# Optimization experiments

Measured on AMD Instinct MI355X. Metric: run time of the kernel, lower is better.

Reference implementation:

```python
import jax, jax.numpy as jnp
import numpy as np

B, P, N, H = 8, 12, 5000, 8
E = 50000
NB = 8
TD0, TD1 = 16, 64
MAX_STEPS = 500


def _proj(x, w1, b1, w2, b2):
    # Projection: Linear -> ReLU -> Linear
    return jax.nn.relu(x @ w1 + b1) @ w2 + b2


def _ln(x, w, b, eps=1e-5):
    # LayerNorm over last two dims [N, H] with affine params [N, H]
    m = jnp.mean(x, axis=(-2, -1), keepdims=True)
    v = jnp.mean((x - m) ** 2, axis=(-2, -1), keepdims=True)
    return (x - m) * jax.lax.rsqrt(v + eps) * w + b


def _time_table():
    # DiffTimeEmbedding buffer: [MAX_STEPS, 2*TD0]
    steps = jnp.arange(MAX_STEPS, dtype=jnp.float32)[:, None]
    dims = jnp.arange(TD0, dtype=jnp.float32)[None, :]
    e = steps * 10.0 ** (dims * 4.0 / TD0)
    return jnp.concatenate([jnp.sin(e), jnp.cos(e)], axis=1)


def setup_inputs() -> dict:
    key = jax.random.key(0)
    ks = jax.random.split(key, 40)
    rn = lambda k, s, sc=0.1: jax.random.normal(k, s, jnp.float32) * sc
    return {
        'x': jax.random.normal(ks[0], (B, P, N), jnp.float32),
        'cond': jax.random.normal(ks[1], (B, P, N, H), jnp.float32),
        'pos': jax.random.normal(ks[2], (N, H), jnp.float32),
        'time': jax.random.randint(ks[3], (B,), 0, MAX_STEPS),
        'edge_index': jax.random.randint(ks[4], (2, E), 0, N),
        'te_w1': rn(ks[5], (2 * TD0, TD1)), 'te_b1': rn(ks[6], (TD1,)),
        'te_w2': rn(ks[7], (TD1, TD1)), 'te_b2': rn(ks[8], (TD1,)),
        'in_w1': rn(ks[9], (1, H)), 'in_b1': rn(ks[10], (H,)),
        'in_w2': rn(ks[11], (H, H)), 'in_b2': rn(ks[12], (H,)),
        'pos_w1': rn(ks[13], (H, H)), 'pos_b1': rn(ks[14], (H,)),
        'pos_w2': rn(ks[15], (H, H)), 'pos_b2': rn(ks[16], (H,)),
        'attn': jax.random.normal(ks[17], (NB + 1, 1), jnp.float32),
        'bt_w1': rn(ks[18], (NB, TD1, H)), 'bt_b1': rn(ks[19], (NB, H)),
        'bt_w2': rn(ks[20], (NB, H, H)), 'bt_b2': rn(ks[21], (NB, H)),
        'bc_w1': rn(ks[22], (NB, H, H)), 'bc_b1': rn(ks[23], (NB, H)),
        'bc_w2': rn(ks[24], (NB, H, H)), 'bc_b2': rn(ks[25], (NB, H)),
        'gn_w': 1.0 + rn(ks[26], (NB, N, H), 0.05), 'gn_b': rn(ks[27], (NB, N, H), 0.05),
        'tn_w': 1.0 + rn(ks[28], (NB, N, H), 0.05), 'tn_b': rn(ks[29], (NB, N, H), 0.05),
        'cv_w': rn(ks[30], (NB, P, P)), 'cv_b': rn(ks[31], (NB, P)),
        'out_w1': rn(ks[32], (H, H)), 'out_b1': rn(ks[33], (H,)),
        'out_w2': rn(ks[34], (H, 1)), 'out_b2': rn(ks[35], (1,)),
    }


def _forward(x, cond, pos, te_w1, te_b1, te_w2, te_b2, in_w1, in_b1, in_w2, in_b2,
             pos_w1, pos_b1, pos_w2, pos_b2, attn, bt_w1, bt_b1, bt_w2, bt_b2,
             bc_w1, bc_b1, bc_w2, bc_b2, gn_w, gn_b, tn_w, tn_b, cv_w, cv_b,
             out_w1, out_b1, out_w2, out_b2, time, edge_index):
    # diffusion-time embedding -> [B, TD1]
    te = _time_table()[time]
    te = jax.nn.silu(te @ te_w1 + te_b1)
    te = jax.nn.silu(te @ te_w2 + te_b2)
    # input + positional projection -> [B, P, N, H]
    h = _proj(x[..., None], in_w1, in_b1, in_w2, in_b2)
    h = h + _proj(pos, pos_w1, pos_b1, pos_w2, pos_b2)
    # LGConv symmetric GCN norm (no self loops), shared across blocks
    src, dst = edge_index[0], edge_index[1]
    deg = jnp.zeros((N,), h.dtype).at[dst].add(1.0)
    dinv = jnp.where(deg > 0, 1.0 / jnp.sqrt(jnp.where(deg > 0, deg, 1.0)), 0.0)
    enorm = dinv[src] * dinv[dst]  # [E]
    skips = [h]
    for i in range(NB):
        t = _proj(te, bt_w1[i], bt_b1[i], bt_w2[i], bt_b2[i])[:, None, None, :]
        c = _proj(cond, bc_w1[i], bc_b1[i], bc_w2[i], bc_b2[i])
        h = _ln(h + c, gn_w[i], gn_b[i])
        # LGConv: gather -> scale -> scatter-add along node dim (-2)
        msg = h[:, :, src, :] * enorm[None, None, :, None]
        h = jnp.zeros_like(h).at[:, :, dst, :].add(msg)
        h = _ln(h + t, tn_w[i], tn_b[i])
        # 1x1 Conv2d over period channels
        h = jnp.einsum('bpnh,qp->bqnh', h, cv_w[i]) + cv_b[i][None, :, None, None]
        skips.append(h)
    s = jnp.stack(skips, axis=-1)  # [B, P, N, H, NB+1]
    a = jax.nn.softmax(attn, axis=0)  # [NB+1, 1]
    h = (s @ a)[..., 0]  # [B, P, N, H]
    return _proj(h, out_w1, out_b1, out_w2, out_b2)[..., 0]  # [B, P, N]


def reference(x, cond, pos, te_w1, te_b1, te_w2, te_b2, in_w1, in_b1, in_w2, in_b2,
              pos_w1, pos_b1, pos_w2, pos_b2, attn, bt_w1, bt_b1, bt_w2, bt_b2,
              bc_w1, bc_b1, bc_w2, bc_b2, gn_w, gn_b, tn_w, tn_b, cv_w, cv_b,
              out_w1, out_b1, out_w2, out_b2, time, edge_index):
    return _forward(x, cond, pos, te_w1, te_b1, te_w2, te_b2, in_w1, in_b1, in_w2, in_b2,
                    pos_w1, pos_b1, pos_w2, pos_b2, attn, bt_w1, bt_b1, bt_w2, bt_b2,
                    bc_w1, bc_b1, bc_w2, bc_b2, gn_w, gn_b, tn_w, tn_b, cv_w, cv_b,
                    out_w1, out_b1, out_w2, out_b2, time, edge_index)
```

## Files before the change

### kernel.cpp

```cpp
#include <hip/hip_runtime.h>
#include <math.h>

#define Bv 8
#define Pv 12
#define Nv 5000
#define Hv 8
#define Ev 50000
#define NBv 8
#define TD1v 64
#define NIMG (Bv * Pv)
#define BLKS_PER_IMG 20
#define ECAP 3072

typedef float f4v __attribute__((ext_vector_type(4)));

__device__ inline float4 nt_load4(const float* p) {
  f4v v = __builtin_nontemporal_load((const f4v*)p);
  return make_float4(v.x, v.y, v.z, v.w);
}
__device__ inline void nt_store4(float* p, float a, float b, float c, float d) {
  f4v v = {a, b, c, d};
  __builtin_nontemporal_store(v, (f4v*)p);
}

__device__ __constant__ float POW10Q[16] = {
  1.0f, 1.7782794100389228f, 3.1622776601683795f, 5.623413251903491f,
  10.0f, 17.78279410038923f, 31.622776601683793f, 56.23413251903491f,
  100.0f, 177.82794100389228f, 316.22776601683796f, 562.341325190349f,
  1000.0f, 1778.2794100389228f, 3162.2776601683795f, 5623.413251903491f
};

__global__ void k_setup(const int* timei, const float* attn,
                        const float* te_w1, const float* te_b1,
                        const float* te_w2, const float* te_b2,
                        const float* bt_w1, const float* bt_b1,
                        const float* bt_w2, const float* bt_b2,
                        float* t_all, float* a9) {
  __shared__ float te0[Bv][32];
  __shared__ float te1[Bv][64];
  __shared__ float te2[Bv][64];
  int t = threadIdx.x;
  for (int idx = t; idx < Bv * 16; idx += 64) {
    int b = idx >> 4, d = idx & 15;
    float e = (float)timei[b] * POW10Q[d];
    te0[b][d]      = (float)sin((double)e);
    te0[b][d + 16] = (float)cos((double)e);
  }
  __syncthreads();
  for (int idx = t; idx < Bv * 64; idx += 64) {
    int b = idx >> 6, j = idx & 63;
    float s = te_b1[j];
    for (int k = 0; k < 32; ++k) s += te0[b][k] * te_w1[k * 64 + j];
    te1[b][j] = s / (1.0f + expf(-s));
  }
  __syncthreads();
  for (int idx = t; idx < Bv * 64; idx += 64) {
    int b = idx >> 6, j = idx & 63;
    float s = te_b2[j];
    for (int k = 0; k < 64; ++k) s += te1[b][k] * te_w2[k * 64 + j];
    te2[b][j] = s / (1.0f + expf(-s));
  }
  __syncthreads();
  {
    int i = t >> 3, b = t & 7;
    float u[Hv];
    for (int j = 0; j < Hv; ++j) {
      float s = bt_b1[i * Hv + j];
      for (int k = 0; k < TD1v; ++k) s += te2[b][k] * bt_w1[(i * TD1v + k) * Hv + j];
      u[j] = fmaxf(s, 0.0f);
    }
    for (int ch = 0; ch < Hv; ++ch) {
      float s = bt_b2[i * Hv + ch];
      for (int j = 0; j < Hv; ++j) s += u[j] * bt_w2[(i * Hv + j) * Hv + ch];
      t_all[(i * Bv + b) * Hv + ch] = s;
    }
  }
  if (t == 0) {
    float m = attn[0];
    for (int i = 1; i < 9; ++i) m = fmaxf(m, attn[i]);
    float s = 0.f, ex[9];
    for (int i = 0; i < 9; ++i) { ex[i] = expf(attn[i] - m); s += ex[i]; }
    for (int i = 0; i < 9; ++i) a9[i] = ex[i] / s;
  }
}

__global__ void k_posp(const float* pos, const float* pw1, const float* pb1,
                       const float* pw2, const float* pb2, float* posp) {
  int n = blockIdx.x * blockDim.x + threadIdx.x;
  if (n >= Nv) return;
  const float4* pr = (const float4*)(pos + (size_t)n * Hv);
  float4 r0 = pr[0], r1 = pr[1];
  float x[8] = {r0.x, r0.y, r0.z, r0.w, r1.x, r1.y, r1.z, r1.w};
  float u[8];
  #pragma unroll
  for (int j = 0; j < 8; ++j) {
    float s = pb1[j];
    #pragma unroll
    for (int k = 0; k < 8; ++k) s += x[k] * pw1[k * 8 + j];
    u[j] = fmaxf(s, 0.f);
  }
  float o[8];
  #pragma unroll
  for (int ch = 0; ch < 8; ++ch) {
    float s = pb2[ch];
    #pragma unroll
    for (int j = 0; j < 8; ++j) s += u[j] * pw2[j * 8 + ch];
    o[ch] = s;
  }
  float4* po = (float4*)(posp + (size_t)n * Hv);
  po[0] = make_float4(o[0], o[1], o[2], o[3]);
  po[1] = make_float4(o[4], o[5], o[6], o[7]);
}

__global__ void k_zero(float* deg, int* cursor, float* stats) {
  int i = blockIdx.x * blockDim.x + threadIdx.x;
  if (i < Nv) { deg[i] = 0.f; cursor[i] = 0; }
  if (i < NBv * 2 * NIMG * 2) stats[i] = 0.f;
}

__global__ void k_deg(const int* eidx, float* deg) {
  int e = blockIdx.x * blockDim.x + threadIdx.x;
  if (e < Ev) atomicAdd(&deg[eidx[Ev + e]], 1.0f);
}

__global__ void k_dinv(const float* deg, float* dinv) {
  int n = blockIdx.x * blockDim.x + threadIdx.x;
  if (n < Nv) {
    float d = deg[n];
    dinv[n] = d > 0.f ? (float)(1.0 / sqrt((double)d)) : 0.f;
  }
}

__global__ void k_scan(const float* deg, int* row_ptr) {
  __shared__ int buf[1024];
  __shared__ int base_s;
  int t = threadIdx.x;
  if (t == 0) { base_s = 0; row_ptr[0] = 0; }
  __syncthreads();
  for (int c = 0; c < 5; ++c) {
    int i = c * 1024 + t;
    int v = (i < Nv) ? (int)(deg[i] + 0.5f) : 0;
    buf[t] = v;
    __syncthreads();
    for (int off = 1; off < 1024; off <<= 1) {
      int add = (t >= off) ? buf[t - off] : 0;
      __syncthreads();
      buf[t] += add;
      __syncthreads();
    }
    int base = base_s;
    if (i < Nv) row_ptr[i + 1] = base + buf[t];
    __syncthreads();
    if (t == 1023) base_s = base + buf[1023];
    __syncthreads();
  }
}

__global__ void k_csr(const int* eidx, const float* dinv, const int* row_ptr,
                      int* cursor, float2* epack) {
  int e = blockIdx.x * blockDim.x + threadIdx.x;
  if (e >= Ev) return;
  int s = eidx[e], d = eidx[Ev + e];
  int slot = atomicAdd(&cursor[d], 1);
  int pos = row_ptr[d] + slot;
  epack[pos] = make_float2(__int_as_float(s), dinv[s] * dinv[d]);
}

__global__ __launch_bounds__(256) void k_gwb(
    const int* __restrict__ row_ptr, const float2* __restrict__ epack,
    const float* __restrict__ gn_w, const float* __restrict__ gn_b,
    float* __restrict__ Gw, float* __restrict__ Gb) {
  int id = blockIdx.x * 256 + threadIdx.x;
  if (id >= NBv * Nv) return;
  int i = id / Nv, n = id % Nv;
  const float* gw = gn_w + (size_t)i * Nv * Hv;
  const float* gb = gn_b + (size_t)i * Nv * Hv;
  float aw[8] = {0,0,0,0,0,0,0,0}, ab[8] = {0,0,0,0,0,0,0,0};
  int e0 = row_ptr[n], e1 = row_ptr[n + 1];
  for (int e = e0; e < e1; ++e) {
    float2 ep = epack[e];
    int s = __float_as_int(ep.x);
    float w = ep.y;
    const float4* wr = (const float4*)(gw + (size_t)s * Hv);
    const float4* br = (const float4*)(gb + (size_t)s * Hv);
    float4 w0 = wr[0], w1 = wr[1], b0 = br[0], b1 = br[1];
    aw[0] += w * w0.x; aw[1] += w * w0.y; aw[2] += w * w0.z; aw[3] += w * w0.w;
    aw[4] += w * w1.x; aw[5] += w * w1.y; aw[6] += w * w1.z; aw[7] += w * w1.w;
    ab[0] += w * b0.x; ab[1] += w * b0.y; ab[2] += w * b0.z; ab[3] += w * b0.w;
    ab[4] += w * b1.x; ab[5] += w * b1.y; ab[6] += w * b1.z; ab[7] += w * b1.w;
  }
  float4* wo = (float4*)(Gw + (size_t)id * Hv);
  wo[0] = make_float4(aw[0], aw[1], aw[2], aw[3]);
  wo[1] = make_float4(aw[4], aw[5], aw[6], aw[7]);
  float4* bo = (float4*)(Gb + (size_t)id * Hv);
  bo[0] = make_float4(ab[0], ab[1], ab[2], ab[3]);
  bo[1] = make_float4(ab[4], ab[5], ab[6], ab[7]);
}

__global__ void k_init(const float* x, const float* posp,
                       const float* iw1, const float* ib1,
                       const float* iw2, const float* ib2,
                       const float* a9, float* hA, float* acc) {
  int t = blockIdx.x * blockDim.x + threadIdx.x;
  if (t >= Bv * Pv * Nv) return;
  float xv = __builtin_nontemporal_load(x + t);
  float u[8];
  #pragma unroll
  for (int j = 0; j < 8; ++j) u[j] = fmaxf(xv * iw1[j] + ib1[j], 0.f);
  int n = t % Nv;
  const float4* pp = (const float4*)(posp + (size_t)n * Hv);
  float4 p0 = pp[0], p1 = pp[1];
  float pv[8] = {p0.x, p0.y, p0.z, p0.w, p1.x, p1.y, p1.z, p1.w};
  float a0 = a9[0];
  float o[8];
  #pragma unroll
  for (int ch = 0; ch < 8; ++ch) {
    float s = ib2[ch];
    #pragma unroll
    for (int j = 0; j < 8; ++j) s += u[j] * iw2[j * 8 + ch];
    o[ch] = s + pv[ch];
  }
  float4* hr = (float4*)(hA + (size_t)t * Hv);
  hr[0] = make_float4(o[0], o[1], o[2], o[3]);
  hr[1] = make_float4(o[4], o[5], o[6], o[7]);
  nt_store4(acc + (size_t)t * Hv,     a0 * o[0], a0 * o[1], a0 * o[2], a0 * o[3]);
  nt_store4(acc + (size_t)t * Hv + 4, a0 * o[4], a0 * o[5], a0 * o[6], a0 * o[7]);
}

__device__ inline void partial_to_stats(float s1, float s2, float* stats_g) {
  #pragma unroll
  for (int off = 32; off > 0; off >>= 1) {
    s1 += __shfl_down(s1, off, 64);
    s2 += __shfl_down(s2, off, 64);
  }
  __shared__ float r1[4], r2[4];
  int wid = threadIdx.x >> 6, lane = threadIdx.x & 63;
  if (lane == 0) { r1[wid] = s1; r2[wid] = s2; }
  __syncthreads();
  if (threadIdx.x == 0) {
    float a = r1[0] + r1[1] + r1[2] + r1[3];
    float b = r2[0] + r2[1] + r2[2] + r2[3];
    atomicAdd(&stats_g[0], a);
    atomicAdd(&stats_g[1], b);
  }
  __syncthreads();
}

__device__ inline void img_swizzle(int bx, int& g, int& chunk) {
  int xcd = bx & 7;
  int local = bx >> 3;
  g = xcd * 12 + local / BLKS_PER_IMG;
  chunk = local % BLKS_PER_IMG;
}

__global__ __launch_bounds__(256) void k_stage1(
    const float* __restrict__ h, const float* __restrict__ cond,
    const float* w1, const float* b1, const float* w2, const float* b2,
    const float* __restrict__ gnw,
    float* __restrict__ vt, float* stats1) {
  __shared__ float lw1[64], lw2[64], lb1[8], lb2[8];
  int t = threadIdx.x;
  if (t < 64) lw1[t] = w1[t];
  else if (t < 128) lw2[t - 64] = w2[t - 64];
  else if (t < 136) lb1[t - 128] = b1[t - 128];
  else if (t < 144) lb2[t - 136] = b2[t - 136];
  __syncthreads();
  int g, chunk;
  img_swizzle(blockIdx.x, g, chunk);
  int n = chunk * 256 + t;
  float s1 = 0.f, s2 = 0.f;
  if (n < Nv) {
    size_t row = ((size_t)g * Nv + n) * Hv;
    float4 c0 = nt_load4(cond + row);
    float4 c1 = nt_load4(cond + row + 4);
    float xc[8] = {c0.x, c0.y, c0.z, c0.w, c1.x, c1.y, c1.z, c1.w};
    float u[8];
    #pragma unroll
    for (int j = 0; j < 8; ++j) {
      float s = lb1[j];
      #pragma unroll
      for (int k = 0; k < 8; ++k) s += xc[k] * lw1[k * 8 + j];
      u[j] = fmaxf(s, 0.f);
    }
    const float4* hr = (const float4*)(h + row);
    float4 h0 = hr[0], h1 = hr[1];
    float hv[8] = {h0.x, h0.y, h0.z, h0.w, h1.x, h1.y, h1.z, h1.w};
    const float4* gr = (const float4*)(gnw + (size_t)n * Hv);
    float4 g0 = gr[0], g1 = gr[1];
    float gv[8] = {g0.x, g0.y, g0.z, g0.w, g1.x, g1.y, g1.z, g1.w};
    float o[8];
    #pragma unroll
    for (int ch = 0; ch < 8; ++ch) {
      float s = lb2[ch];
      #pragma unroll
      for (int j = 0; j < 8; ++j) s += u[j] * lw2[j * 8 + ch];
      float val = s + hv[ch];
      s1 += val; s2 += val * val;
      o[ch] = val * gv[ch];
    }
    float4* vo = (float4*)(vt + row);
    vo[0] = make_float4(o[0], o[1], o[2], o[3]);
    vo[1] = make_float4(o[4], o[5], o[6], o[7]);
  }
  partial_to_stats(s1, s2, stats1 + (size_t)g * 2);
}

__global__ __launch_bounds__(256) void k_stage2(
    const float* __restrict__ vt, float* __restrict__ v2,
    const int* __restrict__ row_ptr, const float2* __restrict__ epack,
    const float* __restrict__ Gw, const float* __restrict__ Gb,
    const float* __restrict__ stats1, float* stats2,
    const float* __restrict__ tvec) {
  __shared__ float2 se[ECAP];
  int t = threadIdx.x;
  int g, chunk;
  img_swizzle(blockIdx.x, g, chunk);
  int b = g / Pv;
  int nb0 = chunk * 256;
  int nb1 = nb0 + 256; if (nb1 > Nv) nb1 = Nv;
  int eb0 = row_ptr[nb0];
  int eb1 = row_ptr[nb1];
  int cnt = eb1 - eb0;
  const float2* eps;
  int ebase;
  if (cnt <= ECAP) {
    for (int k = t; k < cnt; k += 256) se[k] = epack[eb0 + k];
    eps = se; ebase = eb0;
  } else {
    eps = epack; ebase = 0;
  }
  __syncthreads();
  float mean = stats1[g * 2] * (1.f / 40000.f);
  float m2   = stats1[g * 2 + 1] * (1.f / 40000.f);
  float var  = m2 - mean * mean;
  float rstd = (float)(1.0 / sqrt((double)var + 1e-5));
  float mrs  = mean * rstd;
  int n = nb0 + t;
  float s1 = 0.f, s2 = 0.f;
  if (n < Nv) {
    const float* vtb = vt + (size_t)g * Nv * Hv;
    float a8[8] = {0,0,0,0,0,0,0,0};
    int e0 = row_ptr[n] - ebase, e1 = row_ptr[n + 1] - ebase;
    int e = e0;
    for (; e + 4 <= e1; e += 4) {
      float2 p0 = eps[e], p1 = eps[e+1], p2 = eps[e+2], p3 = eps[e+3];
      const float4* r0 = (const float4*)(vtb + (size_t)__float_as_int(p0.x) * Hv);
      const float4* r1 = (const float4*)(vtb + (size_t)__float_as_int(p1.x) * Hv);
      const float4* r2 = (const float4*)(vtb + (size_t)__float_as_int(p2.x) * Hv);
      const float4* r3 = (const float4*)(vtb + (size_t)__float_as_int(p3.x) * Hv);
      float4 x00 = r0[0], x01 = r0[1];
      float4 x10 = r1[0], x11 = r1[1];
      float4 x20 = r2[0], x21 = r2[1];
      float4 x30 = r3[0], x31 = r3[1];
      a8[0] += p0.y*x00.x + p1.y*x10.x + p2.y*x20.x + p3.y*x30.x;
      a8[1] += p0.y*x00.y + p1.y*x10.y + p2.y*x20.y + p3.y*x30.y;
      a8[2] += p0.y*x00.z + p1.y*x10.z + p2.y*x20.z + p3.y*x30.z;
      a8[3] += p0.y*x00.w + p1.y*x10.w + p2.y*x20.w + p3.y*x30.w;
      a8[4] += p0.y*x01.x + p1.y*x11.x + p2.y*x21.x + p3.y*x31.x;
      a8[5] += p0.y*x01.y + p1.y*x11.y + p2.y*x21.y + p3.y*x31.y;
      a8[6] += p0.y*x01.z + p1.y*x11.z + p2.y*x21.z + p3.y*x31.z;
      a8[7] += p0.y*x01.w + p1.y*x11.w + p2.y*x21.w + p3.y*x31.w;
    }
    for (; e < e1; ++e) {
      float2 ep = eps[e];
      float w = ep.y;
      const float4* sr = (const float4*)(vtb + (size_t)__float_as_int(ep.x) * Hv);
      float4 x0 = sr[0], x1 = sr[1];
      a8[0] += w*x0.x; a8[1] += w*x0.y; a8[2] += w*x0.z; a8[3] += w*x0.w;
      a8[4] += w*x1.x; a8[5] += w*x1.y; a8[6] += w*x1.z; a8[7] += w*x1.w;
    }
    size_t noff = (size_t)n * Hv;
    const float4* wr = (const float4*)(Gw + noff);
    const float4* br = (const float4*)(Gb + noff);
    float4 w0 = wr[0], w1 = wr[1], b0 = br[0], b1 = br[1];
    float gw8[8] = {w0.x, w0.y, w0.z, w0.w, w1.x, w1.y, w1.z, w1.w};
    float gb8[8] = {b0.x, b0.y, b0.z, b0.w, b1.x, b1.y, b1.z, b1.w};
    float o[8];
    #pragma unroll
    for (int ch = 0; ch < 8; ++ch) {
      float val = rstd * a8[ch] - mrs * gw8[ch] + gb8[ch] + tvec[b * Hv + ch];
      o[ch] = val;
      s1 += val; s2 += val * val;
    }
    float* vo = v2 + (size_t)g * Nv * Hv + noff;
    nt_store4(vo,     o[0], o[1], o[2], o[3]);
    nt_store4(vo + 4, o[4], o[5], o[6], o[7]);
  }
  partial_to_stats(s1, s2, stats2 + (size_t)g * 2);
}

__global__ __launch_bounds__(256) void k_stage3(
    float* __restrict__ v2, float* __restrict__ acc,
    const float* __restrict__ stats2,
    const float* __restrict__ tnw, const float* __restrict__ tnb,
    const float* __restrict__ cw, const float* __restrict__ cb,
    const float* __restrict__ a9, int iblk) {
  __shared__ float scw[144], scb[12], smean[12], srstd[12];
  int t = threadIdx.x;
  int b = blockIdx.x & 7;
  int chunk = blockIdx.x >> 3;
  if (t < 144) scw[t] = cw[t];
  else if (t < 156) scb[t - 144] = cb[t - 144];
  else if (t < 168) {
    int p = t - 156;
    int g = b * Pv + p;
    float mean = stats2[g * 2] * (1.f / 40000.f);
    float m2   = stats2[g * 2 + 1] * (1.f / 40000.f);
    float var  = m2 - mean * mean;
    smean[p] = mean;
    srstd[p] = (float)(1.0 / sqrt((double)var + 1e-5));
  }
  __syncthreads();
  int idx = chunk * 256 + t;
  if (idx >= Nv * 2) return;
  int n = idx >> 1, c4 = idx & 1;
  size_t noff = (size_t)n * Hv + c4 * 4;
  const float4 w4 = nt_load4(tnw + noff);
  const float4 b4 = nt_load4(tnb + noff);
  size_t strideP = (size_t)Nv * Hv;
  size_t base = (size_t)b * Pv * strideP + noff;
  float4 in[12];
  #pragma unroll
  for (int p = 0; p < 12; ++p) {
    float4 v = nt_load4(v2 + base + p * strideP);
    float mean = smean[p], rstd = srstd[p];
    in[p].x = (v.x - mean) * rstd * w4.x + b4.x;
    in[p].y = (v.y - mean) * rstd * w4.y + b4.y;
    in[p].z = (v.z - mean) * rstd * w4.z + b4.z;
    in[p].w = (v.w - mean) * rstd * w4.w + b4.w;
  }
  float ai = a9[iblk + 1];
  #pragma unroll
  for (int q = 0; q < 12; ++q) {
    float4 o = make_float4(scb[q], scb[q], scb[q], scb[q]);
    #pragma unroll
    for (int p = 0; p < 12; ++p) {
      float c = scw[q * 12 + p];
      o.x += c * in[p].x; o.y += c * in[p].y;
      o.z += c * in[p].z; o.w += c * in[p].w;
    }
    size_t off = base + q * strideP;
    *(float4*)(v2 + off) = o;
    float4 av = nt_load4(acc + off);
    nt_store4(acc + off, av.x + ai * o.x, av.y + ai * o.y,
                         av.z + ai * o.z, av.w + ai * o.w);
  }
}

__global__ void k_out(const float* acc, const float* ow1, const float* ob1,
                      const float* ow2, const float* ob2, float* out) {
  int t = blockIdx.x * blockDim.x + threadIdx.x;
  if (t >= Bv * Pv * Nv) return;
  float4 a0 = nt_load4(acc + (size_t)t * Hv);
  float4 a1 = nt_load4(acc + (size_t)t * Hv + 4);
  float x[8] = {a0.x, a0.y, a0.z, a0.w, a1.x, a1.y, a1.z, a1.w};
  float o = ob2[0];
  #pragma unroll
  for (int j = 0; j < 8; ++j) {
    float s = ob1[j];
    #pragma unroll
    for (int k = 0; k < 8; ++k) s += x[k] * ow1[k * 8 + j];
    o += fmaxf(s, 0.f) * ow2[j];
  }
  out[t] = o;
}

extern "C" void kernel_launch(void* const* d_in, const int* in_sizes, int n_in,
                              void* d_out, int out_size, void* d_ws, size_t ws_size,
                              hipStream_t stream) {
  const float* x      = (const float*)d_in[0];
  const float* cond   = (const float*)d_in[1];
  const float* pos    = (const float*)d_in[2];
  const int*   timei  = (const int*)  d_in[3];
  const int*   eidx   = (const int*)  d_in[4];
  const float* te_w1  = (const float*)d_in[5];
  const float* te_b1  = (const float*)d_in[6];
  const float* te_w2  = (const float*)d_in[7];
  const float* te_b2  = (const float*)d_in[8];
  const float* in_w1  = (const float*)d_in[9];
  const float* in_b1  = (const float*)d_in[10];
  const float* in_w2  = (const float*)d_in[11];
  const float* in_b2  = (const float*)d_in[12];
  const float* pos_w1 = (const float*)d_in[13];
  const float* pos_b1 = (const float*)d_in[14];
  const float* pos_w2 = (const float*)d_in[15];
  const float* pos_b2 = (const float*)d_in[16];
  const float* attn   = (const float*)d_in[17];
  const float* bt_w1  = (const float*)d_in[18];
  const float* bt_b1  = (const float*)d_in[19];
  const float* bt_w2  = (const float*)d_in[20];
  const float* bt_b2  = (const float*)d_in[21];
  const float* bc_w1  = (const float*)d_in[22];
  const float* bc_b1  = (const float*)d_in[23];
  const float* bc_w2  = (const float*)d_in[24];
  const float* bc_b2  = (const float*)d_in[25];
  const float* gn_w   = (const float*)d_in[26];
  const float* gn_b   = (const float*)d_in[27];
  const float* tn_w   = (const float*)d_in[28];
  const float* tn_b   = (const float*)d_in[29];
  const float* cv_w   = (const float*)d_in[30];
  const float* cv_b   = (const float*)d_in[31];
  const float* out_w1 = (const float*)d_in[32];
  const float* out_b1 = (const float*)d_in[33];
  const float* out_w2 = (const float*)d_in[34];
  const float* out_b2 = (const float*)d_in[35];
  float* out = (float*)d_out;

  const size_t HSZ = (size_t)Bv * Pv * Nv * Hv;
  float* ws    = (float*)d_ws;
  float* X     = ws;
  float* Y     = X + HSZ;
  float* acc   = Y + HSZ;
  float* posp  = acc + HSZ;
  float* deg   = posp + Nv * Hv;
  float* dinv  = deg + Nv;
  float* epack = dinv + Nv;
  float* t_all = epack + 2 * Ev;
  float* a9    = t_all + NBv * Bv * Hv;
  float* stats = a9 + 16;
  float* Gw    = stats + NBv * 2 * NIMG * 2;
  float* Gb    = Gw + NBv * Nv * Hv;
  int* row_ptr = (int*)(Gb + NBv * Nv * Hv);
  int* cursor  = row_ptr + Nv + 8;

  k_setup<<<1, 64, 0, stream>>>(timei, attn, te_w1, te_b1, te_w2, te_b2,
                                bt_w1, bt_b1, bt_w2, bt_b2, t_all, a9);
  k_posp<<<(Nv + 255) / 256, 256, 0, stream>>>(pos, pos_w1, pos_b1, pos_w2, pos_b2, posp);
  k_zero<<<(Nv + 255) / 256, 256, 0, stream>>>(deg, cursor, stats);
  k_deg<<<(Ev + 255) / 256, 256, 0, stream>>>(eidx, deg);
  k_dinv<<<(Nv + 255) / 256, 256, 0, stream>>>(deg, dinv);
  k_scan<<<1, 1024, 0, stream>>>(deg, row_ptr);
  k_csr<<<(Ev + 255) / 256, 256, 0, stream>>>(eidx, dinv, row_ptr, cursor, (float2*)epack);
  k_gwb<<<(NBv * Nv + 255) / 256, 256, 0, stream>>>(
      row_ptr, (const float2*)epack, gn_w, gn_b, Gw, Gb);
  k_init<<<(Bv * Pv * Nv + 255) / 256, 256, 0, stream>>>(
      x, posp, in_w1, in_b1, in_w2, in_b2, a9, X, acc);

  for (int i = 0; i < NBv; ++i) {
    float* st1 = stats + (size_t)(i * 2 + 0) * NIMG * 2;
    float* st2 = stats + (size_t)(i * 2 + 1) * NIMG * 2;
    k_stage1<<<NIMG * BLKS_PER_IMG, 256, 0, stream>>>(
        X, cond,
        bc_w1 + i * 64, bc_b1 + i * 8, bc_w2 + i * 64, bc_b2 + i * 8,
        gn_w + (size_t)i * Nv * Hv,
        Y, st1);
    k_stage2<<<NIMG * BLKS_PER_IMG, 256, 0, stream>>>(
        Y, X, row_ptr, (const float2*)epack,
        Gw + (size_t)i * Nv * Hv, Gb + (size_t)i * Nv * Hv,
        st1, st2, t_all + i * Bv * Hv);
    k_stage3<<<8 * 40, 256, 0, stream>>>(
        X, acc, st2,
        tn_w + (size_t)i * Nv * Hv, tn_b + (size_t)i * Nv * Hv,
        cv_w + i * 144, cv_b + i * 12, a9, i);
  }
  k_out<<<(Bv * Pv * Nv + 255) / 256, 256, 0, stream>>>(
      acc, out_w1, out_b1, out_w2, out_b2, out);
}
```

Measured before the change: 639.0 us.

## Process two images per thread in the graph aggregation stage

Each stage2 block now handles two images (period pairs) for the same node chunk, so CSR edge metadata staged in shared memory and row_ptr/Gw/Gb loads are shared across two images. Grid shrinks by half and the inner loop unrolls by 2 edges across 2 images instead of 4 edges for one. This amortizes edge-list loads but halves the number of blocks and raises register pressure per thread, which may reduce parallelism for the latency-bound gather.

```diff
diff --git a/kernel.cpp b/kernel.cpp
--- a/kernel.cpp
+++ b/kernel.cpp
@@ -11,6 +11,7 @@
 #define NIMG (Bv * Pv)
 #define BLKS_PER_IMG 20
 #define ECAP 3072
+#define IPT2 2
 
 typedef float f4v __attribute__((ext_vector_type(4)));
 
@@ -313,9 +314,11 @@
     const float* __restrict__ tvec) {
   __shared__ float2 se[ECAP];
   int t = threadIdx.x;
-  int g, chunk;
-  img_swizzle(blockIdx.x, g, chunk);
-  int b = g / Pv;
+  int b = blockIdx.x & 7;
+  int local = blockIdx.x >> 3;
+  int pair = local % 6;
+  int chunk = local / 6;
+  int g0 = b * Pv + pair * IPT2;
   int nb0 = chunk * 256;
   int nb1 = nb0 + 256; if (nb1 > Nv) nb1 = Nv;
   int eb0 = row_ptr[nb0];
@@ -330,44 +333,71 @@
     eps = epack; ebase = 0;
   }
   __syncthreads();
-  float mean = stats1[g * 2] * (1.f / 40000.f);
-  float m2   = stats1[g * 2 + 1] * (1.f / 40000.f);
-  float var  = m2 - mean * mean;
-  float rstd = (float)(1.0 / sqrt((double)var + 1e-5));
-  float mrs  = mean * rstd;
+  float mean[IPT2], rstd[IPT2], mrs[IPT2];
+  #pragma unroll
+  for (int j = 0; j < IPT2; ++j) {
+    float m  = stats1[(g0 + j) * 2]     * (1.f / 40000.f);
+    float m2 = stats1[(g0 + j) * 2 + 1] * (1.f / 40000.f);
+    float var = m2 - m * m;
+    mean[j] = m;
+    rstd[j] = (float)(1.0 / sqrt((double)var + 1e-5));
+    mrs[j]  = m * rstd[j];
+  }
   int n = nb0 + t;
-  float s1 = 0.f, s2 = 0.f;
+  float s1a[IPT2], s2a[IPT2];
+  #pragma unroll
+  for (int j = 0; j < IPT2; ++j) { s1a[j] = 0.f; s2a[j] = 0.f; }
   if (n < Nv) {
-    const float* vtb = vt + (size_t)g * Nv * Hv;
-    float a8[8] = {0,0,0,0,0,0,0,0};
+    const float* vt0 = vt + (size_t)(g0 + 0) * Nv * Hv;
+    const float* vt1 = vt + (size_t)(g0 + 1) * Nv * Hv;
+    float a[IPT2][8];
+    #pragma unroll
+    for (int j = 0; j < IPT2; ++j)
+      #pragma unroll
+      for (int ch = 0; ch < 8; ++ch) a[j][ch] = 0.f;
     int e0 = row_ptr[n] - ebase, e1 = row_ptr[n + 1] - ebase;
     int e = e0;
-    for (; e + 4 <= e1; e += 4) {
-      float2 p0 = eps[e], p1 = eps[e+1], p2 = eps[e+2], p3 = eps[e+3];
-      const float4* r0 = (const float4*)(vtb + (size_t)__float_as_int(p0.x) * Hv);
-      const float4* r1 = (const float4*)(vtb + (size_t)__float_as_int(p1.x) * Hv);
-      const float4* r2 = (const float4*)(vtb + (size_t)__float_as_int(p2.x) * Hv);
-      const float4* r3 = (const float4*)(vtb + (size_t)__float_as_int(p3.x) * Hv);
-      float4 x00 = r0[0], x01 = r0[1];
-      float4 x10 = r1[0], x11 = r1[1];
-      float4 x20 = r2[0], x21 = r2[1];
-      float4 x30 = r3[0], x31 = r3[1];
-      a8[0] += p0.y*x00.x + p1.y*x10.x + p2.y*x20.x + p3.y*x30.x;
-      a8[1] += p0.y*x00.y + p1.y*x10.y + p2.y*x20.y + p3.y*x30.y;
-      a8[2] += p0.y*x00.z + p1.y*x10.z + p2.y*x20.z + p3.y*x30.z;
-      a8[3] += p0.y*x00.w + p1.y*x10.w + p2.y*x20.w + p3.y*x30.w;
-      a8[4] += p0.y*x01.x + p1.y*x11.x + p2.y*x21.x + p3.y*x31.x;
-      a8[5] += p0.y*x01.y + p1.y*x11.y + p2.y*x21.y + p3.y*x31.y;
-      a8[6] += p0.y*x01.z + p1.y*x11.z + p2.y*x21.z + p3.y*x31.z;
-      a8[7] += p0.y*x01.w + p1.y*x11.w + p2.y*x21.w + p3.y*x31.w;
+    for (; e + 2 <= e1; e += 2) {
+      float2 p0 = eps[e], p1 = eps[e + 1];
+      size_t so0 = (size_t)__float_as_int(p0.x) * Hv;
+      size_t so1 = (size_t)__float_as_int(p1.x) * Hv;
+      const float4* r00 = (const float4*)(vt0 + so0);
+      const float4* r01 = (const float4*)(vt1 + so0);
+      const float4* r10 = (const float4*)(vt0 + so1);
+      const float4* r11 = (const float4*)(vt1 + so1);
+      float4 x00a = r00[0], x00b = r00[1];
+      float4 x01a = r01[0], x01b = r01[1];
+      float4 x10a = r10[0], x10b = r10[1];
+      float4 x11a = r11[0], x11b = r11[1];
+      a[0][0] += p0.y*x00a.x + p1.y*x10a.x;
+      a[0][1] += p0.y*x00a.y + p1.y*x10a.y;
+      a[0][2] += p0.y*x00a.z + p1.y*x10a.z;
+      a[0][3] += p0.y*x00a.w + p1.y*x10a.w;
+      a[0][4] += p0.y*x00b.x + p1.y*x10b.x;
+      a[0][5] += p0.y*x00b.y + p1.y*x10b.y;
+      a[0][6] += p0.y*x00b.z + p1.y*x10b.z;
+      a[0][7] += p0.y*x00b.w + p1.y*x10b.w;
+      a[1][0] += p0.y*x01a.x + p1.y*x11a.x;
+      a[1][1] += p0.y*x01a.y + p1.y*x11a.y;
+      a[1][2] += p0.y*x01a.z + p1.y*x11a.z;
+      a[1][3] += p0.y*x01a.w + p1.y*x11a.w;
+      a[1][4] += p0.y*x01b.x + p1.y*x11b.x;
+      a[1][5] += p0.y*x01b.y + p1.y*x11b.y;
+      a[1][6] += p0.y*x01b.z + p1.y*x11b.z;
+      a[1][7] += p0.y*x01b.w + p1.y*x11b.w;
     }
     for (; e < e1; ++e) {
       float2 ep = eps[e];
       float w = ep.y;
-      const float4* sr = (const float4*)(vtb + (size_t)__float_as_int(ep.x) * Hv);
-      float4 x0 = sr[0], x1 = sr[1];
-      a8[0] += w*x0.x; a8[1] += w*x0.y; a8[2] += w*x0.z; a8[3] += w*x0.w;
-      a8[4] += w*x1.x; a8[5] += w*x1.y; a8[6] += w*x1.z; a8[7] += w*x1.w;
+      size_t so = (size_t)__float_as_int(ep.x) * Hv;
+      const float4* r0 = (const float4*)(vt0 + so);
+      const float4* r1 = (const float4*)(vt1 + so);
+      float4 xa = r0[0], xb = r0[1];
+      float4 ya = r1[0], yb = r1[1];
+      a[0][0] += w*xa.x; a[0][1] += w*xa.y; a[0][2] += w*xa.z; a[0][3] += w*xa.w;
+      a[0][4] += w*xb.x; a[0][5] += w*xb.y; a[0][6] += w*xb.z; a[0][7] += w*xb.w;
+      a[1][0] += w*ya.x; a[1][1] += w*ya.y; a[1][2] += w*ya.z; a[1][3] += w*ya.w;
+      a[1][4] += w*yb.x; a[1][5] += w*yb.y; a[1][6] += w*yb.z; a[1][7] += w*yb.w;
     }
     size_t noff = (size_t)n * Hv;
     const float4* wr = (const float4*)(Gw + noff);
@@ -375,18 +405,30 @@
     float4 w0 = wr[0], w1 = wr[1], b0 = br[0], b1 = br[1];
     float gw8[8] = {w0.x, w0.y, w0.z, w0.w, w1.x, w1.y, w1.z, w1.w};
     float gb8[8] = {b0.x, b0.y, b0.z, b0.w, b1.x, b1.y, b1.z, b1.w};
-    float o[8];
-    #pragma unroll
-    for (int ch = 0; ch < 8; ++ch) {
-      float val = rstd * a8[ch] - mrs * gw8[ch] + gb8[ch] + tvec[b * Hv + ch];
-      o[ch] = val;
-      s1 += val; s2 += val * val;
-    }
-    float* vo = v2 + (size_t)g * Nv * Hv + noff;
-    nt_store4(vo,     o[0], o[1], o[2], o[3]);
-    nt_store4(vo + 4, o[4], o[5], o[6], o[7]);
-  }
-  partial_to_stats(s1, s2, stats2 + (size_t)g * 2);
+    float tl[8];
+    {
+      const float4* tr = (const float4*)(tvec + b * Hv);
+      float4 t0 = tr[0], t1 = tr[1];
+      tl[0] = t0.x; tl[1] = t0.y; tl[2] = t0.z; tl[3] = t0.w;
+      tl[4] = t1.x; tl[5] = t1.y; tl[6] = t1.z; tl[7] = t1.w;
+    }
+    #pragma unroll
+    for (int j = 0; j < IPT2; ++j) {
+      float o[8];
+      #pragma unroll
+      for (int ch = 0; ch < 8; ++ch) {
+        float val = rstd[j] * a[j][ch] - mrs[j] * gw8[ch] + gb8[ch] + tl[ch];
+        o[ch] = val;
+        s1a[j] += val; s2a[j] += val * val;
+      }
+      float* vo = v2 + (size_t)(g0 + j) * Nv * Hv + noff;
+      nt_store4(vo,     o[0], o[1], o[2], o[3]);
+      nt_store4(vo + 4, o[4], o[5], o[6], o[7]);
+    }
+  }
+  #pragma unroll
+  for (int j = 0; j < IPT2; ++j)
+    partial_to_stats(s1a[j], s2a[j], stats2 + (size_t)(g0 + j) * 2);
 }
 
 __global__ __launch_bounds__(256) void k_stage3(
@@ -404,7 +446,7 @@
   else if (t < 168) {
     int p = t - 156;
     int g = b * Pv + p;
-    float mean = stats2[g * 2] * (1.f / 40000.f);
+    float mean = stats2[g * 2]     * (1.f / 40000.f);
     float m2   = stats2[g * 2 + 1] * (1.f / 40000.f);
     float var  = m2 - mean * mean;
     smean[p] = mean;
@@ -544,7 +586,7 @@
         bc_w1 + i * 64, bc_b1 + i * 8, bc_w2 + i * 64, bc_b2 + i * 8,
         gn_w + (size_t)i * Nv * Hv,
         Y, st1);
-    k_stage2<<<NIMG * BLKS_PER_IMG, 256, 0, stream>>>(
+    k_stage2<<<8 * 6 * BLKS_PER_IMG, 256, 0, stream>>>(
         Y, X, row_ptr, (const float2*)epack,
         Gw + (size_t)i * Nv * Hv, Gb + (size_t)i * Nv * Hv,
         st1, st2, t_all + i * Bv * Hv);
```

After: 619.8 us. 3.0% less time.
